# Performance work log

Hardware: AMD Instinct MI355X
Metric: run time of the kernel (lower is better)

Reference implementation:

```python
import jax, jax.numpy as jnp
import numpy as np

IN_F = 3
HID = 256
N_HIDDEN = 4  # number of hidden SineLayers after the first
OUT_F = 3
OMEGA_0 = 30.0
OMEGA_H = 30.0
N_PTS = 262144


def _uniform(key, shape, bound):
    return jax.random.uniform(key, shape, jnp.float32, -bound, bound)


def setup_inputs() -> dict:
    key = jax.random.key(0)
    ks = jax.random.split(key, 8)
    # coordinates in [-1, 1]
    x = jax.random.uniform(ks[0], (N_PTS, IN_F), jnp.float32, -1.0, 1.0)
    # first layer: W ~ U(-1/n, 1/n)
    w_first = _uniform(ks[1], (HID, IN_F), 1.0 / IN_F)
    b_first = _uniform(ks[2], (HID,), 1.0 / np.sqrt(IN_F))
    # hidden layers: W ~ U(-sqrt(6/n)/omega, sqrt(6/n)/omega), stacked for scan
    hb = np.sqrt(6.0 / HID) / OMEGA_H
    w_hidden = _uniform(ks[3], (N_HIDDEN, HID, HID), hb)
    b_hidden = _uniform(ks[4], (N_HIDDEN, HID), 1.0 / np.sqrt(HID))
    # final linear: same SIREN bound with omega=30
    fb = np.sqrt(6.0 / HID) / 30.0
    w_final = _uniform(ks[5], (OUT_F, HID), fb)
    b_final = _uniform(ks[6], (OUT_F,), 1.0 / np.sqrt(HID))
    return {
        "x": x,
        "w_first": w_first,
        "b_first": b_first,
        "w_hidden": w_hidden,
        "b_hidden": b_hidden,
        "w_final": w_final,
        "b_final": b_final,
    }


def reference(x, w_first, b_first, w_hidden, b_hidden, w_final, b_final):
    # first sine layer: sin(omega_0 * (x W^T + b))
    h = jnp.sin(OMEGA_0 * (x @ w_first.T + b_first))

    # hidden sine layers via scan over stacked [L, HID, HID] weights
    def step(h, wb):
        w, b = wb
        return jnp.sin(OMEGA_H * (h @ w.T + b)), None

    h, _ = jax.lax.scan(step, h, (w_hidden, b_hidden))
    # final linear (no activation: final_activation=None)
    return h @ w_final.T + b_final
```

## Files before the change

### kernel.cpp

```cpp
#include <hip/hip_runtime.h>


typedef _Float16 hf8 __attribute__((ext_vector_type(8)));
typedef _Float16 hf4 __attribute__((ext_vector_type(4)));
typedef _Float16 hf2 __attribute__((ext_vector_type(2)));
typedef __fp16   fp16x2 __attribute__((ext_vector_type(2)));
typedef float floatx4 __attribute__((ext_vector_type(4)));

#define HID 256
#define NHID 4
#define BM 64
#define STRIDE 264
#define THREADS 512
#define NP (BM/16)
#define C_REV 4.774648292756860f
#define WH_ELEMS (NHID*HID*HID)
#define WS_HALVES (WH_ELEMS + 3*HID)

__device__ __forceinline__ float sin_rev(float r){
  float f, s;
  asm("v_fract_f32 %0, %1" : "=v"(f) : "v"(r));
  asm("v_sin_f32 %0, %1"   : "=v"(s) : "v"(f));
  return s;
}
__device__ __forceinline__ hf2 pk2(float a, float b){
  const fp16x2 p = __builtin_amdgcn_cvt_pkrtz(a, b);
  return __builtin_bit_cast(hf2, p);
}
__device__ __forceinline__ hf8 ld8h_f32(const float* f){
  const floatx4 a = *(const floatx4*)f;
  const floatx4 b = *(const floatx4*)(f + 4);
  hf8 o;
#pragma unroll
  for (int e = 0; e < 4; ++e){ o[e] = (_Float16)a[e]; o[4+e] = (_Float16)b[e]; }
  return o;
}
__device__ __forceinline__ int hix(int r, int c){ return r*STRIDE + c; }

__global__ void prep_kernel(const float* __restrict__ wh,
                            const float* __restrict__ wfin,
                            _Float16* __restrict__ ws){
  const int i = blockIdx.x*256 + threadIdx.x;
  if (i < WH_ELEMS)            ws[i] = (_Float16)wh[i];
  else if (i < WS_HALVES)      ws[i] = (_Float16)wfin[i - WH_ELEMS];
}

template<bool WS>
__global__ __launch_bounds__(THREADS, 4) void siren_kernel(
    const float* __restrict__ x, const float* __restrict__ w_first,
    const float* __restrict__ b_first, const float* __restrict__ w_hidden,
    const float* __restrict__ b_hidden, const float* __restrict__ w_final,
    const float* __restrict__ b_final, const _Float16* __restrict__ wsh,
    float* __restrict__ out)
{
  __shared__ __align__(16) _Float16 hbuf[2][BM*STRIDE];
  __shared__ __align__(16) float    wf[HID*4];
  __shared__ __align__(16) float    blds[NHID*HID];
  __shared__ __align__(16) _Float16 wflds[3*HID];

  const int tid = threadIdx.x;
  const int blk = blockIdx.x;

  const int wv  = tid >> 6;
  const int l   = tid & 63;
  const int l15 = l & 15;
  const int l4  = l >> 4;

  if (tid < HID){
    wf[tid*4+0] = w_first[tid*3+0] * C_REV;
    wf[tid*4+1] = w_first[tid*3+1] * C_REV;
    wf[tid*4+2] = w_first[tid*3+2] * C_REV;
    wf[tid*4+3] = b_first[tid]     * C_REV;
  }
#pragma unroll
  for (int i = tid; i < NHID*HID; i += THREADS)
    blds[i] = b_hidden[i] * C_REV;
#pragma unroll
  for (int i = tid; i < 3*HID; i += THREADS)
    wflds[i] = WS ? wsh[WH_ELEMS + i] : (_Float16)w_final[i];
  __syncthreads();

  hf8   wfr[2][8];
  float bC[2][4];
#pragma unroll
  for (int m2 = 0; m2 < 2; ++m2){
    const int jrow  = wv*32 + m2*16 + l15;
    const int wbase = jrow*HID + l4*8;
#pragma unroll
    for (int k = 0; k < 8; ++k){
      if (WS) wfr[m2][k] = *(const hf8*)(wsh + wbase + k*32);
      else    wfr[m2][k] = ld8h_f32(w_hidden + wbase + k*32);
    }
    const int j0 = wv*32 + m2*16 + l4*4;
    const floatx4 bb = *(const floatx4*)(&blds[j0]);
#pragma unroll
    for (int g = 0; g < 4; ++g) bC[m2][g] = bb[g];
  }
  __builtin_amdgcn_sched_barrier(0);

  {
    const int row = tid & (BM-1);
    const int cb  = (tid >> 6) * 32;
    const int gr  = blk*BM + row;
    const float x0 = x[gr*3+0];
    const float x1 = x[gr*3+1];
    const float x2 = x[gr*3+2];
#pragma unroll
    for (int g = 0; g < 4; ++g){
      float sv[8];
#pragma unroll
      for (int e = 0; e < 8; ++e){
        const int j = cb + g*8 + e;
        const floatx4 w = *(const floatx4*)(&wf[j*4]);
        float r = w[3];
        r = fmaf(x0, w[0], r);
        r = fmaf(x1, w[1], r);
        r = fmaf(x2, w[2], r);
        sv[e] = sin_rev(r);
      }
      hf8 hv;
#pragma unroll
      for (int p = 0; p < 4; ++p){
        const hf2 pk = pk2(sv[2*p], sv[2*p+1]);
        hv[2*p] = pk[0]; hv[2*p+1] = pk[1];
      }
      *(hf8*)(&hbuf[0][hix(row, cb + g*8)]) = hv;
    }
  }
  __syncthreads();

  float* fred = (float*)&hbuf[0][0];

  const _Float16* rb = &hbuf[0][0];
  _Float16*       wb = &hbuf[1][0];
#pragma unroll 1
  for (int L = 0; L < NHID; ++L){
    const bool last = (L == NHID-1);
#pragma unroll 2
    for (int np = 0; np < NP; ++np){
      const int npr = (np + wv) & 3;
      const int r = npr*16 + l15;
      hf8 bh[8];
#pragma unroll
      for (int k = 0; k < 8; ++k)
        bh[k] = *(const hf8*)(rb + hix(r, k*32 + l4*8));
      floatx4 acc0 = {0.f,0.f,0.f,0.f};
      floatx4 acc1 = {0.f,0.f,0.f,0.f};
#pragma unroll
      for (int k = 0; k < 8; ++k){
        acc0 = __builtin_amdgcn_mfma_f32_16x16x32_f16(wfr[0][k], bh[k], acc0, 0, 0, 0);
        acc1 = __builtin_amdgcn_mfma_f32_16x16x32_f16(wfr[1][k], bh[k], acc1, 0, 0, 0);
      }
      float p0 = 0.f, p1 = 0.f, p2 = 0.f;
#pragma unroll
      for (int m2 = 0; m2 < 2; ++m2){
        const floatx4 z = m2 ? acc1 : acc0;
        float sv[4];
#pragma unroll
        for (int g = 0; g < 4; ++g)
          sv[g] = sin_rev(fmaf(z[g], C_REV, bC[m2][g]));
        const int jb = wv*32 + m2*16 + l4*4;
        if (!last){
          const hf2 q0 = pk2(sv[0], sv[1]);
          const hf2 q1 = pk2(sv[2], sv[3]);
          hf4 hv; hv[0]=q0[0]; hv[1]=q0[1]; hv[2]=q1[0]; hv[3]=q1[1];
          *(hf4*)(wb + hix(r, jb)) = hv;
        } else {
          const hf4 w0 = *(const hf4*)(&wflds[0*HID + jb]);
          const hf4 w1 = *(const hf4*)(&wflds[1*HID + jb]);
          const hf4 w2 = *(const hf4*)(&wflds[2*HID + jb]);
#pragma unroll
          for (int g = 0; g < 4; ++g){
            p0 = fmaf(sv[g], (float)w0[g], p0);
            p1 = fmaf(sv[g], (float)w1[g], p1);
            p2 = fmaf(sv[g], (float)w2[g], p2);
          }
        }
      }
      if (last){
        p0 += __shfl_xor(p0, 16); p0 += __shfl_xor(p0, 32);
        p1 += __shfl_xor(p1, 16); p1 += __shfl_xor(p1, 32);
        p2 += __shfl_xor(p2, 16); p2 += __shfl_xor(p2, 32);
        if (l < 16){
          floatx4 pv = {p0, p1, p2, 0.f};
          *(floatx4*)(&fred[(wv*BM + r)*4]) = pv;
        }
      }
    }

    __builtin_amdgcn_sched_barrier(0);
    if (L + 1 < NHID){
#pragma unroll
      for (int m2 = 0; m2 < 2; ++m2){
        const int jrow  = wv*32 + m2*16 + l15;
        const int wbase = (L+1)*HID*HID + jrow*HID + l4*8;
#pragma unroll
        for (int k = 0; k < 8; ++k){
          if (WS) wfr[m2][k] = *(const hf8*)(wsh + wbase + k*32);
          else    wfr[m2][k] = ld8h_f32(w_hidden + wbase + k*32);
        }
        const int j0 = wv*32 + m2*16 + l4*4;
        const floatx4 bb = *(const floatx4*)(&blds[(L+1)*HID + j0]);
#pragma unroll
        for (int g = 0; g < 4; ++g) bC[m2][g] = bb[g];
      }
    }
    _Float16* t = (_Float16*)rb; rb = wb; wb = t;
    __syncthreads();
  }

  if (tid < BM*4){
    const int pt = tid >> 2;
    const int o  = tid & 3;
    if (o < 3){
      float s = 0.f;
#pragma unroll
      for (int w = 0; w < 8; ++w)
        s += fred[(w*BM + pt)*4 + o];
      out[(blk*BM + pt)*3 + o] = s + b_final[o];
    }
  }
}

extern "C" void kernel_launch(void* const* d_in, const int* in_sizes, int n_in,
                              void* d_out, int out_size, void* d_ws, size_t ws_size,
                              hipStream_t stream) {
  const float* x        = (const float*)d_in[0];
  const float* w_first  = (const float*)d_in[1];
  const float* b_first  = (const float*)d_in[2];
  const float* w_hidden = (const float*)d_in[3];
  const float* b_hidden = (const float*)d_in[4];
  const float* w_final  = (const float*)d_in[5];
  const float* b_final  = (const float*)d_in[6];
  float* out = (float*)d_out;
  _Float16* wsh = (_Float16*)d_ws;

  const int npts = in_sizes[0] / 3;
  const int grid = npts / BM;
  const bool use_ws = (ws_size >= (size_t)WS_HALVES * sizeof(_Float16));

  if (use_ws){
    const int pgrid = (WS_HALVES + 255) / 256;
    hipLaunchKernelGGL(prep_kernel, dim3(pgrid), dim3(256), 0, stream,
                       w_hidden, w_final, wsh);
    hipLaunchKernelGGL(siren_kernel<true>, dim3(grid), dim3(THREADS), 0, stream,
                       x, w_first, b_first, w_hidden, b_hidden, w_final, b_final,
                       wsh, out);
  } else {
    hipLaunchKernelGGL(siren_kernel<false>, dim3(grid), dim3(THREADS), 0, stream,
                       x, w_first, b_first, w_hidden, b_hidden, w_final, b_final,
                       wsh, out);
  }
}
```

Baseline: 257.7 us.

## Process multiple point chunks per block with persistent-style chunk loop

Each block now loops over eight 64-point chunks instead of one, shrinking the grid by eight. Per-block setup of first-layer weights, biases and final weights in shared memory is amortised across chunks. Next-chunk coordinates and the first layer's weights are prefetched at the end of each chunk. The risk is fewer blocks than available slots on the GPU, which lowers occupancy and the ability to hide latency.

```diff
diff --git a/kernel.cpp b/kernel.cpp
--- a/kernel.cpp
+++ b/kernel.cpp
@@ -10,6 +10,7 @@
 #define HID 256
 #define NHID 4
 #define BM 64
+#define CHUNKS 8
 #define STRIDE 264
 #define THREADS 512
 #define NP (BM/16)
@@ -61,10 +62,11 @@
   const int tid = threadIdx.x;
   const int blk = blockIdx.x;
 
-  const int wv  = tid >> 6;
-  const int l   = tid & 63;
-  const int l15 = l & 15;
-  const int l4  = l >> 4;
+  const int wv   = tid >> 6;
+  const int l    = tid & 63;
+  const int l15  = l & 15;
+  const int l4   = l >> 4;
+  const int row0 = tid & (BM-1);
 
   if (tid < HID){
     wf[tid*4+0] = w_first[tid*3+0] * C_REV;
@@ -78,7 +80,9 @@
 #pragma unroll
   for (int i = tid; i < 3*HID; i += THREADS)
     wflds[i] = WS ? wsh[WH_ELEMS + i] : (_Float16)w_final[i];
-  __syncthreads();
+
+  int gr = (blk*CHUNKS)*BM + row0;
+  float xc0 = x[gr*3+0], xc1 = x[gr*3+1], xc2 = x[gr*3+2];
 
   hf8   wfr[2][8];
   float bC[2][4];
@@ -97,128 +101,134 @@
     for (int g = 0; g < 4; ++g) bC[m2][g] = bb[g];
   }
   __builtin_amdgcn_sched_barrier(0);
-
-  {
-    const int row = tid & (BM-1);
-    const int cb  = (tid >> 6) * 32;
-    const int gr  = blk*BM + row;
-    const float x0 = x[gr*3+0];
-    const float x1 = x[gr*3+1];
-    const float x2 = x[gr*3+2];
-#pragma unroll
-    for (int g = 0; g < 4; ++g){
-      float sv[8];
-#pragma unroll
-      for (int e = 0; e < 8; ++e){
-        const int j = cb + g*8 + e;
-        const floatx4 w = *(const floatx4*)(&wf[j*4]);
-        float r = w[3];
-        r = fmaf(x0, w[0], r);
-        r = fmaf(x1, w[1], r);
-        r = fmaf(x2, w[2], r);
-        sv[e] = sin_rev(r);
-      }
-      hf8 hv;
-#pragma unroll
-      for (int p = 0; p < 4; ++p){
-        const hf2 pk = pk2(sv[2*p], sv[2*p+1]);
-        hv[2*p] = pk[0]; hv[2*p+1] = pk[1];
-      }
-      *(hf8*)(&hbuf[0][hix(row, cb + g*8)]) = hv;
-    }
-  }
   __syncthreads();
 
   float* fred = (float*)&hbuf[0][0];
 
-  const _Float16* rb = &hbuf[0][0];
-  _Float16*       wb = &hbuf[1][0];
 #pragma unroll 1
-  for (int L = 0; L < NHID; ++L){
-    const bool last = (L == NHID-1);
+  for (int c = 0; c < CHUNKS; ++c){
+    {
+      const int cb = (tid >> 6) * 32;
+#pragma unroll
+      for (int g = 0; g < 4; ++g){
+        float sv[8];
+#pragma unroll
+        for (int e = 0; e < 8; ++e){
+          const int j = cb + g*8 + e;
+          const floatx4 w = *(const floatx4*)(&wf[j*4]);
+          float r = w[3];
+          r = fmaf(xc0, w[0], r);
+          r = fmaf(xc1, w[1], r);
+          r = fmaf(xc2, w[2], r);
+          sv[e] = sin_rev(r);
+        }
+        hf8 hv;
+#pragma unroll
+        for (int p = 0; p < 4; ++p){
+          const hf2 pk = pk2(sv[2*p], sv[2*p+1]);
+          hv[2*p] = pk[0]; hv[2*p+1] = pk[1];
+        }
+        *(hf8*)(&hbuf[0][hix(row0, cb + g*8)]) = hv;
+      }
+    }
+    __syncthreads();
+
+    const _Float16* rb = &hbuf[0][0];
+    _Float16*       wb = &hbuf[1][0];
+#pragma unroll 1
+    for (int L = 0; L < NHID; ++L){
+      const bool last = (L == NHID-1);
 #pragma unroll 2
-    for (int np = 0; np < NP; ++np){
-      const int npr = (np + wv) & 3;
-      const int r = npr*16 + l15;
-      hf8 bh[8];
-#pragma unroll
-      for (int k = 0; k < 8; ++k)
-        bh[k] = *(const hf8*)(rb + hix(r, k*32 + l4*8));
-      floatx4 acc0 = {0.f,0.f,0.f,0.f};
-      floatx4 acc1 = {0.f,0.f,0.f,0.f};
-#pragma unroll
-      for (int k = 0; k < 8; ++k){
-        acc0 = __builtin_amdgcn_mfma_f32_16x16x32_f16(wfr[0][k], bh[k], acc0, 0, 0, 0);
-        acc1 = __builtin_amdgcn_mfma_f32_16x16x32_f16(wfr[1][k], bh[k], acc1, 0, 0, 0);
-      }
-      float p0 = 0.f, p1 = 0.f, p2 = 0.f;
-#pragma unroll
-      for (int m2 = 0; m2 < 2; ++m2){
-        const floatx4 z = m2 ? acc1 : acc0;
-        float sv[4];
-#pragma unroll
-        for (int g = 0; g < 4; ++g)
-          sv[g] = sin_rev(fmaf(z[g], C_REV, bC[m2][g]));
-        const int jb = wv*32 + m2*16 + l4*4;
-        if (!last){
-          const hf2 q0 = pk2(sv[0], sv[1]);
-          const hf2 q1 = pk2(sv[2], sv[3]);
-          hf4 hv; hv[0]=q0[0]; hv[1]=q0[1]; hv[2]=q1[0]; hv[3]=q1[1];
-          *(hf4*)(wb + hix(r, jb)) = hv;
-        } else {
-          const hf4 w0 = *(const hf4*)(&wflds[0*HID + jb]);
-          const hf4 w1 = *(const hf4*)(&wflds[1*HID + jb]);
-          const hf4 w2 = *(const hf4*)(&wflds[2*HID + jb]);
-#pragma unroll
-          for (int g = 0; g < 4; ++g){
-            p0 = fmaf(sv[g], (float)w0[g], p0);
-            p1 = fmaf(sv[g], (float)w1[g], p1);
-            p2 = fmaf(sv[g], (float)w2[g], p2);
+      for (int np = 0; np < NP; ++np){
+        const int npr = (np + wv) & 3;
+        const int r = npr*16 + l15;
+        hf8 bh[8];
+#pragma unroll
+        for (int k = 0; k < 8; ++k)
+          bh[k] = *(const hf8*)(rb + hix(r, k*32 + l4*8));
+        floatx4 acc0 = {0.f,0.f,0.f,0.f};
+        floatx4 acc1 = {0.f,0.f,0.f,0.f};
+#pragma unroll
+        for (int k = 0; k < 8; ++k){
+          acc0 = __builtin_amdgcn_mfma_f32_16x16x32_f16(wfr[0][k], bh[k], acc0, 0, 0, 0);
+          acc1 = __builtin_amdgcn_mfma_f32_16x16x32_f16(wfr[1][k], bh[k], acc1, 0, 0, 0);
+        }
+        float p0 = 0.f, p1 = 0.f, p2 = 0.f;
+#pragma unroll
+        for (int m2 = 0; m2 < 2; ++m2){
+          const floatx4 z = m2 ? acc1 : acc0;
+          float sv[4];
+#pragma unroll
+          for (int g = 0; g < 4; ++g)
+            sv[g] = sin_rev(fmaf(z[g], C_REV, bC[m2][g]));
+          const int jb = wv*32 + m2*16 + l4*4;
+          if (!last){
+            const hf2 q0 = pk2(sv[0], sv[1]);
+            const hf2 q1 = pk2(sv[2], sv[3]);
+            hf4 hv; hv[0]=q0[0]; hv[1]=q0[1]; hv[2]=q1[0]; hv[3]=q1[1];
+            *(hf4*)(wb + hix(r, jb)) = hv;
+          } else {
+            const hf4 w0 = *(const hf4*)(&wflds[0*HID + jb]);
+            const hf4 w1 = *(const hf4*)(&wflds[1*HID + jb]);
+            const hf4 w2 = *(const hf4*)(&wflds[2*HID + jb]);
+#pragma unroll
+            for (int g = 0; g < 4; ++g){
+              p0 = fmaf(sv[g], (float)w0[g], p0);
+              p1 = fmaf(sv[g], (float)w1[g], p1);
+              p2 = fmaf(sv[g], (float)w2[g], p2);
+            }
           }
         }
-      }
-      if (last){
-        p0 += __shfl_xor(p0, 16); p0 += __shfl_xor(p0, 32);
-        p1 += __shfl_xor(p1, 16); p1 += __shfl_xor(p1, 32);
-        p2 += __shfl_xor(p2, 16); p2 += __shfl_xor(p2, 32);
-        if (l < 16){
-          floatx4 pv = {p0, p1, p2, 0.f};
-          *(floatx4*)(&fred[(wv*BM + r)*4]) = pv;
-        }
-      }
-    }
-
-    __builtin_amdgcn_sched_barrier(0);
-    if (L + 1 < NHID){
-#pragma unroll
-      for (int m2 = 0; m2 < 2; ++m2){
-        const int jrow  = wv*32 + m2*16 + l15;
-        const int wbase = (L+1)*HID*HID + jrow*HID + l4*8;
-#pragma unroll
-        for (int k = 0; k < 8; ++k){
-          if (WS) wfr[m2][k] = *(const hf8*)(wsh + wbase + k*32);
-          else    wfr[m2][k] = ld8h_f32(w_hidden + wbase + k*32);
-        }
-        const int j0 = wv*32 + m2*16 + l4*4;
-        const floatx4 bb = *(const floatx4*)(&blds[(L+1)*HID + j0]);
-#pragma unroll
-        for (int g = 0; g < 4; ++g) bC[m2][g] = bb[g];
-      }
-    }
-    _Float16* t = (_Float16*)rb; rb = wb; wb = t;
+        if (last){
+          p0 += __shfl_xor(p0, 16); p0 += __shfl_xor(p0, 32);
+          p1 += __shfl_xor(p1, 16); p1 += __shfl_xor(p1, 32);
+          p2 += __shfl_xor(p2, 16); p2 += __shfl_xor(p2, 32);
+          if (l < 16){
+            floatx4 pv = {p0, p1, p2, 0.f};
+            *(floatx4*)(&fred[(wv*BM + r)*4]) = pv;
+          }
+        }
+      }
+
+      __builtin_amdgcn_sched_barrier(0);
+      const bool more = (L + 1 < NHID) || (c + 1 < CHUNKS);
+      if (more){
+        const int Ln = (L + 1) & (NHID - 1);
+#pragma unroll
+        for (int m2 = 0; m2 < 2; ++m2){
+          const int jrow  = wv*32 + m2*16 + l15;
+          const int wbase = Ln*HID*HID + jrow*HID + l4*8;
+#pragma unroll
+          for (int k = 0; k < 8; ++k){
+            if (WS) wfr[m2][k] = *(const hf8*)(wsh + wbase + k*32);
+            else    wfr[m2][k] = ld8h_f32(w_hidden + wbase + k*32);
+          }
+          const int j0 = wv*32 + m2*16 + l4*4;
+          const floatx4 bb = *(const floatx4*)(&blds[Ln*HID + j0]);
+#pragma unroll
+          for (int g = 0; g < 4; ++g) bC[m2][g] = bb[g];
+        }
+      }
+      if (last && (c + 1 < CHUNKS)){
+        const int grn = (blk*CHUNKS + c + 1)*BM + row0;
+        xc0 = x[grn*3+0]; xc1 = x[grn*3+1]; xc2 = x[grn*3+2];
+      }
+      _Float16* t = (_Float16*)rb; rb = wb; wb = t;
+      __syncthreads();
+    }
+
+    if (tid < BM*4){
+      const int pt = tid >> 2;
+      const int o  = tid & 3;
+      if (o < 3){
+        float s = 0.f;
+#pragma unroll
+        for (int w = 0; w < 8; ++w)
+          s += fred[(w*BM + pt)*4 + o];
+        out[((blk*CHUNKS + c)*BM + pt)*3 + o] = s + b_final[o];
+      }
+    }
     __syncthreads();
-  }
-
-  if (tid < BM*4){
-    const int pt = tid >> 2;
-    const int o  = tid & 3;
-    if (o < 3){
-      float s = 0.f;
-#pragma unroll
-      for (int w = 0; w < 8; ++w)
-        s += fred[(w*BM + pt)*4 + o];
-      out[(blk*BM + pt)*3 + o] = s + b_final[o];
-    }
   }
 }
 
@@ -236,7 +246,7 @@
   _Float16* wsh = (_Float16*)d_ws;
 
   const int npts = in_sizes[0] / 3;
-  const int grid = npts / BM;
+  const int grid = npts / (BM * CHUNKS);
   const bool use_ws = (ws_size >= (size_t)WS_HALVES * sizeof(_Float16));
 
   if (use_ws){
```

After: 316.7 us. +22.9%, slower.

## Halve row tile and stream hidden weights from global to raise occupancy

Applied to the files above, without the earlier changes.

The block tile shrinks from 64 to 32 points, and the launch bound rises to 8 blocks per CU. Hidden-layer weights are no longer held in registers and prefetched across layers. Instead each block streams them from global memory inside the k-loop and computes a 2x2 grid of MFMA tiles, and the first-layer weight table is aliased into the second activation buffer to save LDS. The goal is lower register and LDS use so more waves can hide latency. The cost is twice as many blocks each re-reading the full weight set through L2, with weight loads now sitting directly on the MFMA critical path.

```diff
diff --git a/kernel.cpp b/kernel.cpp
--- a/kernel.cpp
+++ b/kernel.cpp
@@ -9,10 +9,9 @@
 
 #define HID 256
 #define NHID 4
-#define BM 64
+#define BM 32
 #define STRIDE 264
 #define THREADS 512
-#define NP (BM/16)
 #define C_REV 4.774648292756860f
 #define WH_ELEMS (NHID*HID*HID)
 #define WS_HALVES (WH_ELEMS + 3*HID)
@@ -46,7 +45,7 @@
 }
 
 template<bool WS>
-__global__ __launch_bounds__(THREADS, 4) void siren_kernel(
+__global__ __launch_bounds__(THREADS, 8) void siren_kernel(
     const float* __restrict__ x, const float* __restrict__ w_first,
     const float* __restrict__ b_first, const float* __restrict__ w_hidden,
     const float* __restrict__ b_hidden, const float* __restrict__ w_final,
@@ -54,9 +53,9 @@
     float* __restrict__ out)
 {
   __shared__ __align__(16) _Float16 hbuf[2][BM*STRIDE];
-  __shared__ __align__(16) float    wf[HID*4];
   __shared__ __align__(16) float    blds[NHID*HID];
   __shared__ __align__(16) _Float16 wflds[3*HID];
+  float* wf = (float*)&hbuf[1][0];
 
   const int tid = threadIdx.x;
   const int blk = blockIdx.x;
@@ -80,33 +79,15 @@
     wflds[i] = WS ? wsh[WH_ELEMS + i] : (_Float16)w_final[i];
   __syncthreads();
 
-  hf8   wfr[2][8];
-  float bC[2][4];
-#pragma unroll
-  for (int m2 = 0; m2 < 2; ++m2){
-    const int jrow  = wv*32 + m2*16 + l15;
-    const int wbase = jrow*HID + l4*8;
-#pragma unroll
-    for (int k = 0; k < 8; ++k){
-      if (WS) wfr[m2][k] = *(const hf8*)(wsh + wbase + k*32);
-      else    wfr[m2][k] = ld8h_f32(w_hidden + wbase + k*32);
-    }
-    const int j0 = wv*32 + m2*16 + l4*4;
-    const floatx4 bb = *(const floatx4*)(&blds[j0]);
-#pragma unroll
-    for (int g = 0; g < 4; ++g) bC[m2][g] = bb[g];
-  }
-  __builtin_amdgcn_sched_barrier(0);
-
   {
     const int row = tid & (BM-1);
-    const int cb  = (tid >> 6) * 32;
+    const int cb  = (tid >> 5) * 16;
     const int gr  = blk*BM + row;
     const float x0 = x[gr*3+0];
     const float x1 = x[gr*3+1];
     const float x2 = x[gr*3+2];
 #pragma unroll
-    for (int g = 0; g < 4; ++g){
+    for (int g = 0; g < 2; ++g){
       float sv[8];
 #pragma unroll
       for (int e = 0; e < 8; ++e){
@@ -136,25 +117,46 @@
 #pragma unroll 1
   for (int L = 0; L < NHID; ++L){
     const bool last = (L == NHID-1);
-#pragma unroll 2
-    for (int np = 0; np < NP; ++np){
-      const int npr = (np + wv) & 3;
-      const int r = npr*16 + l15;
-      hf8 bh[8];
-#pragma unroll
-      for (int k = 0; k < 8; ++k)
-        bh[k] = *(const hf8*)(rb + hix(r, k*32 + l4*8));
-      floatx4 acc0 = {0.f,0.f,0.f,0.f};
-      floatx4 acc1 = {0.f,0.f,0.f,0.f};
-#pragma unroll
-      for (int k = 0; k < 8; ++k){
-        acc0 = __builtin_amdgcn_mfma_f32_16x16x32_f16(wfr[0][k], bh[k], acc0, 0, 0, 0);
-        acc1 = __builtin_amdgcn_mfma_f32_16x16x32_f16(wfr[1][k], bh[k], acc1, 0, 0, 0);
-      }
+    float bC[2][4];
+#pragma unroll
+    for (int m2 = 0; m2 < 2; ++m2){
+      const floatx4 bb = *(const floatx4*)(&blds[L*HID + wv*32 + m2*16 + l4*4]);
+#pragma unroll
+      for (int g = 0; g < 4; ++g) bC[m2][g] = bb[g];
+    }
+
+    floatx4 a00 = {0.f,0.f,0.f,0.f};
+    floatx4 a10 = {0.f,0.f,0.f,0.f};
+    floatx4 a01 = {0.f,0.f,0.f,0.f};
+    floatx4 a11 = {0.f,0.f,0.f,0.f};
+
+    const _Float16* wp0h = wsh + L*HID*HID + (wv*32 + l15)*HID + l4*8;
+    const float*    wp0f = w_hidden + L*HID*HID + (wv*32 + l15)*HID + l4*8;
+#pragma unroll
+    for (int k = 0; k < 8; ++k){
+      hf8 w0, w1;
+      if (WS){
+        w0 = *(const hf8*)(wp0h + k*32);
+        w1 = *(const hf8*)(wp0h + 16*HID + k*32);
+      } else {
+        w0 = ld8h_f32(wp0f + k*32);
+        w1 = ld8h_f32(wp0f + 16*HID + k*32);
+      }
+      const hf8 b0 = *(const hf8*)(rb + hix(l15,      k*32 + l4*8));
+      const hf8 b1 = *(const hf8*)(rb + hix(16 + l15, k*32 + l4*8));
+      a00 = __builtin_amdgcn_mfma_f32_16x16x32_f16(w0, b0, a00, 0, 0, 0);
+      a10 = __builtin_amdgcn_mfma_f32_16x16x32_f16(w1, b0, a10, 0, 0, 0);
+      a01 = __builtin_amdgcn_mfma_f32_16x16x32_f16(w0, b1, a01, 0, 0, 0);
+      a11 = __builtin_amdgcn_mfma_f32_16x16x32_f16(w1, b1, a11, 0, 0, 0);
+    }
+
+#pragma unroll
+    for (int np = 0; np < 2; ++np){
+      const int r = np*16 + l15;
       float p0 = 0.f, p1 = 0.f, p2 = 0.f;
 #pragma unroll
       for (int m2 = 0; m2 < 2; ++m2){
-        const floatx4 z = m2 ? acc1 : acc0;
+        const floatx4 z = np ? (m2 ? a11 : a01) : (m2 ? a10 : a00);
         float sv[4];
 #pragma unroll
         for (int g = 0; g < 4; ++g)
@@ -187,24 +189,6 @@
         }
       }
     }
-
-    __builtin_amdgcn_sched_barrier(0);
-    if (L + 1 < NHID){
-#pragma unroll
-      for (int m2 = 0; m2 < 2; ++m2){
-        const int jrow  = wv*32 + m2*16 + l15;
-        const int wbase = (L+1)*HID*HID + jrow*HID + l4*8;
-#pragma unroll
-        for (int k = 0; k < 8; ++k){
-          if (WS) wfr[m2][k] = *(const hf8*)(wsh + wbase + k*32);
-          else    wfr[m2][k] = ld8h_f32(w_hidden + wbase + k*32);
-        }
-        const int j0 = wv*32 + m2*16 + l4*4;
-        const floatx4 bb = *(const floatx4*)(&blds[(L+1)*HID + j0]);
-#pragma unroll
-        for (int g = 0; g < 4; ++g) bC[m2][g] = bb[g];
-      }
-    }
     _Float16* t = (_Float16*)rb; rb = wb; wb = t;
     __syncthreads();
   }
```

After: 467.4 us. 81.4% more time.
